# Performance work log

Hardware: AMD Instinct MI355X
Metric: run time of the kernel (lower is better)

Reference implementation:

```python
import jax, jax.numpy as jnp
import numpy as np

DIM = 1024
NUM_HEADS = 16
HEAD_DIM = DIM // NUM_HEADS
FF = 4 * DIM
B, T, S = 8, 512, 4096


def setup_inputs() -> dict:
    key = jax.random.key(0)
    ks = jax.random.split(key, 14)
    sc = 1.0 / np.sqrt(DIM)
    inp = {
        "x": jax.random.normal(ks[0], (B, T, DIM), jnp.float32),
        "inp": jax.random.normal(ks[1], (B, S, DIM), jnp.float32),
        # attention projections
        "Wq": jax.random.normal(ks[2], (DIM, DIM), jnp.float32) * sc,
        "bq": jnp.zeros((DIM,), jnp.float32),
        "Wk": jax.random.normal(ks[3], (DIM, DIM), jnp.float32) * sc,
        "bk": jnp.zeros((DIM,), jnp.float32),
        "Wv": jax.random.normal(ks[4], (DIM, DIM), jnp.float32) * sc,
        "bv": jnp.zeros((DIM,), jnp.float32),
        "Wo": jax.random.normal(ks[5], (DIM, DIM), jnp.float32) * sc,
        "bo": jnp.zeros((DIM,), jnp.float32),
        # MLP
        "W1": jax.random.normal(ks[6], (DIM, FF), jnp.float32) * sc,
        "b1": jnp.zeros((FF,), jnp.float32),
        "W2": jax.random.normal(ks[7], (FF, DIM), jnp.float32) * (1.0 / np.sqrt(FF)),
        "b2": jnp.zeros((DIM,), jnp.float32),
    }
    return inp


def _perceiver_layer(x, inp, Wq, bq, Wk, bk, Wv, bv, Wo, bo, W1, b1, W2, b2):
    b, t, _ = x.shape
    s = inp.shape[1]
    q = (x @ Wq + bq).reshape(b, t, NUM_HEADS, HEAD_DIM)
    k = (inp @ Wk + bk).reshape(b, s, NUM_HEADS, HEAD_DIM)
    v = (inp @ Wv + bv).reshape(b, s, NUM_HEADS, HEAD_DIM)
    # [b, h, t, s] score tensor (as in original code)
    attn = jnp.einsum('bthd,bshd->bhts', q, k)
    attn = jax.nn.softmax(attn / jnp.sqrt(jnp.float32(HEAD_DIM)), axis=-1)
    out = jnp.einsum('bhts,bshd->bthd', attn, v).reshape(b, t, DIM)
    attn_out = out @ Wo + bo
    x = x + attn_out
    h = jax.nn.gelu(x @ W1 + b1, approximate=True)  # flax nn.gelu default is tanh approx
    x = x + (h @ W2 + b2)
    return x


def reference(x, inp, Wq, bq, Wk, bk, Wv, bv, Wo, bo, W1, b1, W2, b2):
    return _perceiver_layer(x, inp, Wq, bq, Wk, bk, Wv, bv, Wo, bo, W1, b1, W2, b2)
```

## Files before the change

kernel.cpp:

```cpp
#include <hip/hip_runtime.h>
#include <hip/hip_bf16.h>

#define DIM 1024
#define NHEADS 16
#define HDIM 64
#define FF_ 4096
#define BB 8
#define TT 512
#define SS 4096

typedef __attribute__((ext_vector_type(8))) __bf16 bf16x8;
typedef __attribute__((ext_vector_type(4))) float f32x4;
typedef __attribute__((ext_vector_type(4))) unsigned short us4;

#define SWZ(r, b) ((b) ^ (((r) & 7) << 4))

typedef const __attribute__((address_space(1))) void gvoid_t;
typedef __attribute__((address_space(3))) void lvoid_t;

__device__ __forceinline__ void ldst16(const void* g, void* l) {
  __builtin_amdgcn_global_load_lds((gvoid_t*)g, (lvoid_t*)l, 16, 0, 0);
}

__device__ inline unsigned short f2bf(float f) {
  unsigned u = __float_as_uint(f);
  u += 0x7fff + ((u >> 16) & 1);
  return (unsigned short)(u >> 16);
}

__device__ __forceinline__ unsigned cvt_pk(float lo, float hi) {
  unsigned r;
  asm("v_cvt_pk_bf16_f32 %0, %1, %2" : "=v"(r) : "v"(lo), "v"(hi));
  return r;
}

__global__ void prep_kernel(const float* __restrict__ x,
                            const float* __restrict__ inp,
                            const float* __restrict__ Wq,
                            const float* __restrict__ Wk,
                            const float* __restrict__ Wv,
                            const float* __restrict__ Wo,
                            const float* __restrict__ W1,
                            const float* __restrict__ W2,
                            const float* __restrict__ bk,
                            const float* __restrict__ bv,
                            unsigned short* __restrict__ xb,
                            unsigned short* __restrict__ inpb,
                            unsigned short* __restrict__ Wqt,
                            unsigned short* __restrict__ Wkvt,
                            unsigned short* __restrict__ Wot,
                            unsigned short* __restrict__ W1t,
                            unsigned short* __restrict__ W2t,
                            float* __restrict__ bkv) {
  __shared__ float tile[32][33];
  const int bid = blockIdx.x, tid = threadIdx.x;

  if (bid < 2048) {
    const int n4 = BB * SS * DIM / 4;
    for (int i = bid * 256 + tid; i < n4; i += 2048 * 256) {
      float4 v = ((const float4*)inp)[i];
      uint2 w = {cvt_pk(v.x, v.y), cvt_pk(v.z, v.w)};
      ((uint2*)inpb)[i] = w;
    }
    return;
  }
  if (bid < 2304) {
    const int n4 = BB * TT * DIM / 4;
    for (int i = (bid - 2048) * 256 + tid; i < n4; i += 256 * 256) {
      float4 v = ((const float4*)x)[i];
      uint2 w = {cvt_pk(v.x, v.y), cvt_pk(v.z, v.w)};
      ((uint2*)xb)[i] = w;
    }
    return;
  }
  if (bid < 14592) {
    const float* in;
    unsigned short* outp;
    int R, C, t, tilesx;
    if (bid < 3328)       { in = Wq; outp = Wqt; R = 1024; C = 1024; t = bid - 2304; tilesx = 32; }
    else if (bid < 4352)  { in = Wk; outp = Wkvt; R = 1024; C = 1024; t = bid - 3328; tilesx = 32; }
    else if (bid < 5376)  { in = Wv; outp = Wkvt + 1024 * 1024; R = 1024; C = 1024; t = bid - 4352; tilesx = 32; }
    else if (bid < 6400)  { in = Wo; outp = Wot; R = 1024; C = 1024; t = bid - 5376; tilesx = 32; }
    else if (bid < 10496) { in = W1; outp = W1t; R = 1024; C = 4096; t = bid - 6400; tilesx = 128; }
    else                  { in = W2; outp = W2t; R = 4096; C = 1024; t = bid - 10496; tilesx = 32; }
    int bc = (t % tilesx) * 32, br = (t / tilesx) * 32;
    int tx = tid & 31, ty = tid >> 5;
#pragma unroll
    for (int i = 0; i < 32; i += 8)
      tile[ty + i][tx] = in[(size_t)(br + ty + i) * C + bc + tx];
    __syncthreads();
#pragma unroll
    for (int i = 0; i < 32; i += 8)
      outp[(size_t)(bc + ty + i) * R + br + tx] = f2bf(tile[tx][ty + i]);
    return;
  }
  for (int i = tid; i < 1024; i += 256) {
    bkv[i] = bk[i];
    bkv[1024 + i] = bv[i];
  }
}

template <int EPI>
__global__ __launch_bounds__(256, 3)
void gemm_kernel(const unsigned short* __restrict__ A,
                 const unsigned short* __restrict__ Bt,
                 const float* __restrict__ bias,
                 const float* __restrict__ res,
                 void* __restrict__ Cp,
                 unsigned short* __restrict__ C2,
                 int M, int N, int K) {
  __shared__ char smem[32768];
  char* As = smem;
  char* Bs = smem + 16384;

  const int tid = threadIdx.x;
  const int lane = tid & 63;
  const int wave = tid >> 6;
  const int wm = wave >> 1, wn = wave & 1;

  const int flat = blockIdx.y * gridDim.x + blockIdx.x;
  const int cpx = (gridDim.x * gridDim.y) >> 3;
  const int swz = (flat & 7) * cpx + (flat >> 3);
  const int m0 = (swz / gridDim.x) * 128, n0 = (swz % gridDim.x) * 128;

  f32x4 acc[4][4];
#pragma unroll
  for (int i = 0; i < 4; ++i)
#pragma unroll
    for (int j = 0; j < 4; ++j) acc[i][j] = (f32x4){0.f, 0.f, 0.f, 0.f};

  for (int k0 = 0; k0 < K; k0 += 64) {
    __syncthreads();
#pragma unroll
    for (int i = 0; i < 4; ++i) {
      int ch = (wave * 4 + i) * 64 + lane;
      int r = ch >> 3, c8 = (ch & 7) ^ (r & 7);
      ldst16(A + (size_t)(m0 + r) * K + k0 + c8 * 8, As + (wave * 4 + i) * 1024);
      ldst16(Bt + (size_t)(n0 + r) * K + k0 + c8 * 8, Bs + (wave * 4 + i) * 1024);
    }
    __syncthreads();

#pragma unroll
    for (int kk = 0; kk < 2; ++kk) {
      bf16x8 a[4], b[4];
#pragma unroll
      for (int mi = 0; mi < 4; ++mi) {
        int r = wm * 64 + mi * 16 + (lane & 15);
        a[mi] = *(const bf16x8*)(As + r * 128 + SWZ(r, kk * 64 + (lane >> 4) * 16));
      }
#pragma unroll
      for (int ni = 0; ni < 4; ++ni) {
        int r = wn * 64 + ni * 16 + (lane & 15);
        b[ni] = *(const bf16x8*)(Bs + r * 128 + SWZ(r, kk * 64 + (lane >> 4) * 16));
      }
#pragma unroll
      for (int mi = 0; mi < 4; ++mi)
#pragma unroll
        for (int ni = 0; ni < 4; ++ni)
          acc[mi][ni] = __builtin_amdgcn_mfma_f32_16x16x32_bf16(b[ni], a[mi], acc[mi][ni], 0, 0, 0);
    }
  }

  const int q = lane & 15, g4 = (lane >> 4) * 4;
#pragma unroll
  for (int mi = 0; mi < 4; ++mi) {
    int row = m0 + wm * 64 + mi * 16 + q;
#pragma unroll
    for (int ni = 0; ni < 4; ++ni) {
      int colb = n0 + wn * 64 + ni * 16 + g4;
      float4 bv = *(const float4*)(bias + colb);
      f32x4 v = acc[mi][ni];
      float v0 = v[0] + bv.x, v1 = v[1] + bv.y, v2 = v[2] + bv.z, v3 = v[3] + bv.w;
      if (EPI == 0) {
        uint2 w = {cvt_pk(v0, v1), cvt_pk(v2, v3)};
        *(uint2*)((unsigned short*)Cp + (size_t)row * N + colb) = w;
      } else if (EPI == 1) {
        float o[4] = {v0, v1, v2, v3};
#pragma unroll
        for (int j = 0; j < 4; ++j) {
          float u = 0.7978845608028654f * (o[j] + 0.044715f * o[j] * o[j] * o[j]);
          float e = __expf(2.f * u);
          float th = 1.f - 2.f / (e + 1.f);
          o[j] = 0.5f * o[j] * (1.f + th);
        }
        uint2 w = {cvt_pk(o[0], o[1]), cvt_pk(o[2], o[3])};
        *(uint2*)((unsigned short*)Cp + (size_t)row * N + colb) = w;
      } else {
        float4 r4 = *(const float4*)(res + (size_t)row * N + colb);
        float o0 = v0 + r4.x, o1 = v1 + r4.y, o2 = v2 + r4.z, o3 = v3 + r4.w;
        float4 ov = {o0, o1, o2, o3};
        *(float4*)((float*)Cp + (size_t)row * N + colb) = ov;
        if (EPI == 3) {
          uint2 w = {cvt_pk(o0, o1), cvt_pk(o2, o3)};
          *(uint2*)(C2 + (size_t)row * N + colb) = w;
        }
      }
    }
  }
}

template <int EPI>
__global__ __launch_bounds__(512, 2)
void gemm256(const unsigned short* __restrict__ A,
             const unsigned short* __restrict__ Bt,
             const float* __restrict__ bias,
             void* __restrict__ Cp,
             unsigned short* __restrict__ C2,
             int M, int N, int K) {
  __shared__ char smem[131072];

  const int tid = threadIdx.x, lane = tid & 63, wave = tid >> 6;
  const int q = lane & 15, g = lane >> 4;
  const int wm = wave >> 2, wn = wave & 3;

  const int flat = blockIdx.y * gridDim.x + blockIdx.x;
  const int cpx = (gridDim.x * gridDim.y) >> 3;
  const int swz = (flat & 7) * cpx + (flat >> 3);
  const int m0 = (swz / gridDim.x) * 256, n0 = (swz % gridDim.x) * 256;

  const unsigned short* Arow = A + (size_t)m0 * K;
  const unsigned short* Brow = Bt + (size_t)n0 * K;

  const int r0 = tid >> 3, c0 = ((tid & 7) ^ (r0 & 7)) * 8;
  const int r1 = (tid + 512) >> 3, c1 = (((tid + 512) & 7) ^ (r1 & 7)) * 8;

#define STA(buf, half, kt)                                                     \
  { char* d = smem + (buf) * 32768 + (half) * 16384;                           \
    const unsigned short* s = Arow + (size_t)((half) * 128) * K + (kt) * 64;   \
    ldst16(s + (size_t)r0 * K + c0, d + tid * 16);                             \
    ldst16(s + (size_t)r1 * K + c1, d + 8192 + tid * 16); }
#define STB(buf, half, kt)                                                     \
  { char* d = smem + 65536 + (buf) * 32768 + (half) * 16384;                   \
    const unsigned short* s = Brow + (size_t)((half) * 128) * K + (kt) * 64;   \
    ldst16(s + (size_t)r0 * K + c0, d + tid * 16);                             \
    ldst16(s + (size_t)r1 * K + c1, d + 8192 + tid * 16); }

  f32x4 acc[8][4];
#pragma unroll
  for (int i = 0; i < 8; ++i)
#pragma unroll
    for (int j = 0; j < 4; ++j) acc[i][j] = (f32x4){0.f, 0.f, 0.f, 0.f};

  STA(0, 0, 0); STA(0, 1, 0); STB(0, 0, 0); STB(0, 1, 0);
  STB(1, 0, 1); STB(1, 1, 1);
  asm volatile("s_waitcnt vmcnt(4)" ::: "memory");
  __builtin_amdgcn_s_barrier();

  const int NKT = K >> 6;
  for (int kt = 0; kt < NKT; ++kt) {
    const int cb = kt & 1, nb = cb ^ 1;
    const char* Ab = smem + cb * 32768;
    const char* Bb = smem + 65536 + cb * 32768;
    bf16x8 bfr[4][2];

#pragma unroll
    for (int p = 0; p < 4; ++p) {
      bf16x8 af[2][2];
#pragma unroll
      for (int i = 0; i < 2; ++i)
#pragma unroll
        for (int kk = 0; kk < 2; ++kk) {
          int r = wm * 128 + (2 * p + i) * 16 + q;
          af[i][kk] = *(const bf16x8*)(Ab + r * 128 + SWZ(r, kk * 64 + g * 16));
        }
      if (p == 0) {
#pragma unroll
        for (int nr = 0; nr < 4; ++nr)
#pragma unroll
          for (int kk = 0; kk < 2; ++kk) {
            int r = wn * 64 + nr * 16 + q;
            bfr[nr][kk] = *(const bf16x8*)(Bb + r * 128 + SWZ(r, kk * 64 + g * 16));
          }
      }

      if (p == 0)      { if (kt + 1 < NKT) { STA(nb, 0, kt + 1); STA(nb, 1, kt + 1); } }
      else if (p == 1) { if (kt + 2 < NKT) STB(cb, 0, kt + 2); }
      else if (p == 2) { if (kt + 2 < NKT) STB(cb, 1, kt + 2); }

      __builtin_amdgcn_s_barrier();
      __builtin_amdgcn_s_setprio(1);
#pragma unroll
      for (int i = 0; i < 2; ++i)
#pragma unroll
        for (int nr = 0; nr < 4; ++nr)
#pragma unroll
          for (int kk = 0; kk < 2; ++kk)
            acc[2 * p + i][nr] = __builtin_amdgcn_mfma_f32_16x16x32_bf16(
                bfr[nr][kk], af[i][kk], acc[2 * p + i][nr], 0, 0, 0);
      __builtin_amdgcn_s_setprio(0);

      if (p == 3) {
        if (kt + 2 < NKT) { asm volatile("s_waitcnt vmcnt(4)" ::: "memory"); }
        else              { asm volatile("s_waitcnt vmcnt(0)" ::: "memory"); }
      }
      __builtin_amdgcn_s_barrier();
    }
  }

  const int g4 = g * 4;
#pragma unroll
  for (int mr = 0; mr < 8; ++mr) {
    int row = m0 + wm * 128 + mr * 16 + q;
#pragma unroll
    for (int nr = 0; nr < 4; ++nr) {
      int colb = n0 + wn * 64 + nr * 16 + g4;
      float4 bv = *(const float4*)(bias + colb);
      f32x4 v = acc[mr][nr];
      float v0 = v[0] + bv.x, v1 = v[1] + bv.y, v2 = v[2] + bv.z, v3 = v[3] + bv.w;
      if (EPI == 1) {
        float o[4] = {v0, v1, v2, v3};
#pragma unroll
        for (int j = 0; j < 4; ++j) {
          float u = 0.7978845608028654f * (o[j] + 0.044715f * o[j] * o[j] * o[j]);
          float e = __expf(2.f * u);
          float th = 1.f - 2.f / (e + 1.f);
          o[j] = 0.5f * o[j] * (1.f + th);
        }
        uint2 w = {cvt_pk(o[0], o[1]), cvt_pk(o[2], o[3])};
        *(uint2*)((unsigned short*)Cp + (size_t)row * N + colb) = w;
      } else {
        if (n0 < 1024) {
          uint2 w = {cvt_pk(v0, v1), cvt_pk(v2, v3)};
          *(uint2*)((unsigned short*)Cp + (size_t)row * 1024 + colb) = w;
        } else {
          int b = row >> 12, s = row & 4095;
          int d0 = colb - 1024;
          unsigned short* vt = C2 + ((size_t)b * DIM + d0) * SS + s;
          vt[0] = f2bf(v0);
          vt[SS] = f2bf(v1);
          vt[2 * SS] = f2bf(v2);
          vt[3 * SS] = f2bf(v3);
        }
      }
    }
  }
#undef STA
#undef STB
}

__global__ __launch_bounds__(256, 2)
void attn_kernel6(const unsigned short* __restrict__ Qb,
                  const unsigned short* __restrict__ Kb,
                  const unsigned short* __restrict__ Vt,
                  unsigned short* __restrict__ Ob) {
  __shared__ char smem[65536];

  const int tid = threadIdx.x, lane = tid & 63, wave = tid >> 6;
  const int bid = blockIdx.x;
  const int b = bid & 7, qt = (bid >> 3) & 3, h = bid >> 5;
  const int q0 = qt * 128;
  const int q = lane & 15, g = lane >> 4;

  const int rA = tid >> 3;
  const int cA = (tid & 7) ^ (rA & 7);
  char* const Pw = smem + 49152 + wave * 4096;

  const unsigned short* srcQ = Qb + ((size_t)b * TT + q0) * DIM + h * HDIM;
  const unsigned short* srcK = Kb + (size_t)b * SS * DIM + h * HDIM;
  const unsigned short* srcV = Vt + ((size_t)b * DIM + h * HDIM) * SS;

  bf16x8 qf0[2], qf1[2];
  {
    const unsigned short* qr0 = srcQ + (size_t)(wave * 32 + q) * DIM;
    const unsigned short* qr1 = srcQ + (size_t)(wave * 32 + 16 + q) * DIM;
    qf0[0] = *(const bf16x8*)(qr0 + g * 8);
    qf0[1] = *(const bf16x8*)(qr0 + 32 + g * 8);
    qf1[0] = *(const bf16x8*)(qr1 + g * 8);
    qf1[1] = *(const bf16x8*)(qr1 + 32 + g * 8);
  }

#define STKV(t, buf)                                                                        \
  { ldst16(srcK + (size_t)((t) * 64 + rA) * DIM + cA * 8, smem + (buf) * 8192 + tid * 16);  \
    ldst16(srcK + (size_t)((t) * 64 + rA + 32) * DIM + cA * 8,                              \
           smem + (buf) * 8192 + 4096 + tid * 16);                                          \
    ldst16(srcV + (size_t)rA * SS + (t) * 64 + cA * 8,                                      \
           smem + 24576 + (buf) * 8192 + tid * 16);                                         \
    ldst16(srcV + (size_t)(rA + 32) * SS + (t) * 64 + cA * 8,                               \
           smem + 24576 + (buf) * 8192 + 4096 + tid * 16); }

  STKV(0, 0);
  STKV(1, 1);
  asm volatile("s_waitcnt vmcnt(4)" ::: "memory");
  __builtin_amdgcn_s_barrier();

  f32x4 acc0[4], acc1[4];
#pragma unroll
  for (int dt = 0; dt < 4; ++dt) {
    acc0[dt] = (f32x4){0.f, 0.f, 0.f, 0.f};
    acc1[dt] = (f32x4){0.f, 0.f, 0.f, 0.f};
  }
  float lsum0 = 0.f, lsum1 = 0.f;
  const float CSC = 0.125f * 1.4426950408889634f;

  const int NT = SS / 64;
  int cur = 0, sb = 2;
  for (int t = 0; t < NT; ++t) {
    char* Kc = smem + cur * 8192;
    char* Vc = smem + 24576 + cur * 8192;
    if (t + 2 < NT) STKV(t + 2, sb);

    f32x4 st0[4], st1[4];
#pragma unroll
    for (int si = 0; si < 4; ++si) {
      st0[si] = (f32x4){0.f, 0.f, 0.f, 0.f};
      st1[si] = (f32x4){0.f, 0.f, 0.f, 0.f};
    }
    __builtin_amdgcn_s_setprio(1);
#pragma unroll
    for (int kk = 0; kk < 2; ++kk)
#pragma unroll
      for (int si = 0; si < 4; ++si) {
        int r = si * 16 + q;
        bf16x8 kf = *(const bf16x8*)(Kc + r * 128 + SWZ(r, kk * 64 + g * 16));
        st0[si] = __builtin_amdgcn_mfma_f32_16x16x32_bf16(kf, qf0[kk], st0[si], 0, 0, 0);
        st1[si] = __builtin_amdgcn_mfma_f32_16x16x32_bf16(kf, qf1[kk], st1[si], 0, 0, 0);
      }
    __builtin_amdgcn_s_setprio(0);

    float rs0 = 0.f, rs1 = 0.f;
#pragma unroll
    for (int si = 0; si < 4; ++si) {
      float a0 = __builtin_amdgcn_exp2f(st0[si][0] * CSC);
      float a1 = __builtin_amdgcn_exp2f(st0[si][1] * CSC);
      float a2 = __builtin_amdgcn_exp2f(st0[si][2] * CSC);
      float a3 = __builtin_amdgcn_exp2f(st0[si][3] * CSC);
      rs0 += (a0 + a1) + (a2 + a3);
      uint2 w0 = {cvt_pk(a0, a1), cvt_pk(a2, a3)};
      *(uint2*)(Pw + q * 128 + SWZ(q, si * 32 + g * 8)) = w0;
      float b0 = __builtin_amdgcn_exp2f(st1[si][0] * CSC);
      float b1 = __builtin_amdgcn_exp2f(st1[si][1] * CSC);
      float b2 = __builtin_amdgcn_exp2f(st1[si][2] * CSC);
      float b3 = __builtin_amdgcn_exp2f(st1[si][3] * CSC);
      rs1 += (b0 + b1) + (b2 + b3);
      uint2 w1 = {cvt_pk(b0, b1), cvt_pk(b2, b3)};
      *(uint2*)(Pw + 2048 + q * 128 + SWZ(q, si * 32 + g * 8)) = w1;
    }
    lsum0 += rs0;
    lsum1 += rs1;

    __builtin_amdgcn_s_setprio(1);
#pragma unroll
    for (int kk = 0; kk < 2; ++kk) {
      bf16x8 pb0 = *(const bf16x8*)(Pw + q * 128 + SWZ(q, kk * 64 + g * 16));
      bf16x8 pb1 = *(const bf16x8*)(Pw + 2048 + q * 128 + SWZ(q, kk * 64 + g * 16));
#pragma unroll
      for (int dt = 0; dt < 4; ++dt) {
        int r = dt * 16 + q;
        bf16x8 va = *(const bf16x8*)(Vc + r * 128 + SWZ(r, kk * 64 + g * 16));
        acc0[dt] = __builtin_amdgcn_mfma_f32_16x16x32_bf16(va, pb0, acc0[dt], 0, 0, 0);
        acc1[dt] = __builtin_amdgcn_mfma_f32_16x16x32_bf16(va, pb1, acc1[dt], 0, 0, 0);
      }
    }
    __builtin_amdgcn_s_setprio(0);

    if (t + 2 < NT) { asm volatile("s_waitcnt vmcnt(4)" ::: "memory"); }
    else            { asm volatile("s_waitcnt vmcnt(0)" ::: "memory"); }
    __builtin_amdgcn_s_barrier();
    cur = cur == 2 ? 0 : cur + 1;
    sb  = sb  == 2 ? 0 : sb  + 1;
  }
#undef STKV

  lsum0 += __shfl_xor(lsum0, 16);
  lsum0 += __shfl_xor(lsum0, 32);
  lsum1 += __shfl_xor(lsum1, 16);
  lsum1 += __shfl_xor(lsum1, 32);
  float inv0 = 1.0f / lsum0, inv1 = 1.0f / lsum1;
#pragma unroll
  for (int dt = 0; dt < 4; ++dt) {
    f32x4 v0 = acc0[dt];
    uint2 w0 = {cvt_pk(v0[0] * inv0, v0[1] * inv0), cvt_pk(v0[2] * inv0, v0[3] * inv0)};
    *(uint2*)(Pw + q * 128 + SWZ(q, dt * 32 + g * 8)) = w0;
    f32x4 v1 = acc1[dt];
    uint2 w1 = {cvt_pk(v1[0] * inv1, v1[1] * inv1), cvt_pk(v1[2] * inv1, v1[3] * inv1)};
    *(uint2*)(Pw + 2048 + q * 128 + SWZ(q, dt * 32 + g * 8)) = w1;
  }
  __builtin_amdgcn_s_waitcnt(0);
  int qr = lane >> 2, cb = (lane & 3) * 32;
  {
    uint4 lo = *(const uint4*)(Pw + qr * 128 + SWZ(qr, cb));
    uint4 hi = *(const uint4*)(Pw + qr * 128 + SWZ(qr, cb + 16));
    size_t ob = ((size_t)b * TT + q0 + wave * 32 + qr) * DIM + h * HDIM + (lane & 3) * 16;
    *(uint4*)(Ob + ob) = lo;
    *(uint4*)(Ob + ob + 8) = hi;
  }
  {
    uint4 lo = *(const uint4*)(Pw + 2048 + qr * 128 + SWZ(qr, cb));
    uint4 hi = *(const uint4*)(Pw + 2048 + qr * 128 + SWZ(qr, cb + 16));
    size_t ob = ((size_t)b * TT + q0 + wave * 32 + 16 + qr) * DIM + h * HDIM + (lane & 3) * 16;
    *(uint4*)(Ob + ob) = lo;
    *(uint4*)(Ob + ob + 8) = hi;
  }
}

extern "C" void kernel_launch(void* const* d_in, const int* in_sizes, int n_in,
                              void* d_out, int out_size, void* d_ws, size_t ws_size,
                              hipStream_t stream) {
  const float* x   = (const float*)d_in[0];
  const float* inp = (const float*)d_in[1];
  const float* Wq  = (const float*)d_in[2];
  const float* bq  = (const float*)d_in[3];
  const float* Wk  = (const float*)d_in[4];
  const float* bk  = (const float*)d_in[5];
  const float* Wv  = (const float*)d_in[6];
  const float* bv  = (const float*)d_in[7];
  const float* Wo  = (const float*)d_in[8];
  const float* bo  = (const float*)d_in[9];
  const float* W1  = (const float*)d_in[10];
  const float* b1  = (const float*)d_in[11];
  const float* W2  = (const float*)d_in[12];
  const float* b2  = (const float*)d_in[13];
  float* out = (float*)d_out;

  char* ws = (char*)d_ws;
  const size_t MB = 1024ull * 1024ull;
  unsigned short* Wqt  = (unsigned short*)(ws + 0 * MB);
  unsigned short* Wkvt = (unsigned short*)(ws + 2 * MB);
  unsigned short* Wot  = (unsigned short*)(ws + 6 * MB);
  unsigned short* W1t  = (unsigned short*)(ws + 8 * MB);
  unsigned short* W2t  = (unsigned short*)(ws + 16 * MB);
  float*          bkv  = (float*)(ws + 24 * MB);
  unsigned short* Qb   = (unsigned short*)(ws + 25 * MB);
  unsigned short* Kb   = (unsigned short*)(ws + 33 * MB);
  float*          x2   = (float*)(ws + 33 * MB);
  unsigned short* x2b  = (unsigned short*)(ws + 49 * MB);
  unsigned short* hb   = (unsigned short*)(ws + 57 * MB);
  unsigned short* Vt   = (unsigned short*)(ws + 97 * MB);
  unsigned short* inpb = (unsigned short*)(ws + 161 * MB);
  unsigned short* xb   = (unsigned short*)(ws + 225 * MB);
  unsigned short* Obf  = (unsigned short*)d_out;

  prep_kernel<<<dim3(14593), 256, 0, stream>>>(x, inp, Wq, Wk, Wv, Wo, W1, W2,
                                               bk, bv, xb, inpb, Wqt, Wkvt,
                                               Wot, W1t, W2t, bkv);

  gemm_kernel<0><<<dim3(8, 32), 256, 0, stream>>>(xb, Wqt, bq, nullptr, Qb, nullptr, BB * TT, DIM, DIM);
  gemm256<2><<<dim3(8, 128), 512, 0, stream>>>(inpb, Wkvt, bkv, Kb, Vt, BB * SS, 2048, DIM);

  attn_kernel6<<<dim3(512), 256, 0, stream>>>(Qb, Kb, Vt, Obf);

  gemm_kernel<3><<<dim3(8, 32), 256, 0, stream>>>(Obf, Wot, bo, x, x2, x2b, BB * TT, DIM, DIM);
  gemm256<1><<<dim3(16, 16), 512, 0, stream>>>(x2b, W1t, b1, hb, nullptr, BB * TT, FF_, DIM);
  gemm_kernel<2><<<dim3(8, 32), 256, 0, stream>>>(hb, W2t, b2, x2, out, nullptr, BB * TT, DIM, FF_);
}
```

Baseline: 452.7 us.

## Switch attention kernel to 32x32x16 MFMA with register-resident P via lane shuffles

The attention kernel now uses 32x32x16 bf16 MFMA tiles instead of 16x16x32 for both QK^T and PV. The exponentiated scores are packed in registers and exchanged across half-waves with shuffles to form the PV operand, so P no longer round-trips through LDS each tile. This is meant to cut LDS traffic, LDS reads and MFMA instruction count per tile. In exchange it adds cross-lane shuffles and selects in the inner loop, and relies on the 32x32 accumulator layout matching the operand layout.

Result: no change. 459.6 us (+1.5%).

```diff
diff --git a/kernel.cpp b/kernel.cpp
--- a/kernel.cpp
+++ b/kernel.cpp
@@ -11,6 +11,7 @@
 
 typedef __attribute__((ext_vector_type(8))) __bf16 bf16x8;
 typedef __attribute__((ext_vector_type(4))) float f32x4;
+typedef __attribute__((ext_vector_type(16))) float f32x16;
 typedef __attribute__((ext_vector_type(4))) unsigned short us4;
 
 #define SWZ(r, b) ((b) ^ (((r) & 7) << 4))
@@ -339,7 +340,7 @@
 }
 
 __global__ __launch_bounds__(256, 2)
-void attn_kernel6(const unsigned short* __restrict__ Qb,
+void attn_kernel7(const unsigned short* __restrict__ Qb,
                   const unsigned short* __restrict__ Kb,
                   const unsigned short* __restrict__ Vt,
                   unsigned short* __restrict__ Ob) {
@@ -349,7 +350,9 @@
   const int bid = blockIdx.x;
   const int b = bid & 7, qt = (bid >> 3) & 3, h = bid >> 5;
   const int q0 = qt * 128;
-  const int q = lane & 15, g = lane >> 4;
+  const int q = lane & 31;
+  const bool hi = lane >= 32;
+  const int ho16 = hi ? 16 : 0;
 
   const int rA = tid >> 3;
   const int cA = (tid & 7) ^ (rA & 7);
@@ -359,14 +362,11 @@
   const unsigned short* srcK = Kb + (size_t)b * SS * DIM + h * HDIM;
   const unsigned short* srcV = Vt + ((size_t)b * DIM + h * HDIM) * SS;
 
-  bf16x8 qf0[2], qf1[2];
+  bf16x8 qf[4];
   {
-    const unsigned short* qr0 = srcQ + (size_t)(wave * 32 + q) * DIM;
-    const unsigned short* qr1 = srcQ + (size_t)(wave * 32 + 16 + q) * DIM;
-    qf0[0] = *(const bf16x8*)(qr0 + g * 8);
-    qf0[1] = *(const bf16x8*)(qr0 + 32 + g * 8);
-    qf1[0] = *(const bf16x8*)(qr1 + g * 8);
-    qf1[1] = *(const bf16x8*)(qr1 + 32 + g * 8);
+    const unsigned short* qrow = srcQ + (size_t)(wave * 32 + q) * DIM + (hi ? 8 : 0);
+#pragma unroll
+    for (int dt = 0; dt < 4; ++dt) qf[dt] = *(const bf16x8*)(qrow + dt * 16);
   }
 
 #define STKV(t, buf)                                                                        \
@@ -383,13 +383,10 @@
   asm volatile("s_waitcnt vmcnt(4)" ::: "memory");
   __builtin_amdgcn_s_barrier();
 
-  f32x4 acc0[4], acc1[4];
-#pragma unroll
-  for (int dt = 0; dt < 4; ++dt) {
-    acc0[dt] = (f32x4){0.f, 0.f, 0.f, 0.f};
-    acc1[dt] = (f32x4){0.f, 0.f, 0.f, 0.f};
-  }
-  float lsum0 = 0.f, lsum1 = 0.f;
+  f32x16 oa0, oa1;
+#pragma unroll
+  for (int i = 0; i < 16; ++i) { oa0[i] = 0.f; oa1[i] = 0.f; }
+  float lsum = 0.f;
   const float CSC = 0.125f * 1.4426950408889634f;
 
   const int NT = SS / 64;
@@ -399,57 +396,56 @@
     char* Vc = smem + 24576 + cur * 8192;
     if (t + 2 < NT) STKV(t + 2, sb);
 
-    f32x4 st0[4], st1[4];
-#pragma unroll
-    for (int si = 0; si < 4; ++si) {
-      st0[si] = (f32x4){0.f, 0.f, 0.f, 0.f};
-      st1[si] = (f32x4){0.f, 0.f, 0.f, 0.f};
-    }
+    f32x16 sa0, sa1;
+#pragma unroll
+    for (int i = 0; i < 16; ++i) { sa0[i] = 0.f; sa1[i] = 0.f; }
     __builtin_amdgcn_s_setprio(1);
 #pragma unroll
-    for (int kk = 0; kk < 2; ++kk)
-#pragma unroll
-      for (int si = 0; si < 4; ++si) {
-        int r = si * 16 + q;
-        bf16x8 kf = *(const bf16x8*)(Kc + r * 128 + SWZ(r, kk * 64 + g * 16));
-        st0[si] = __builtin_amdgcn_mfma_f32_16x16x32_bf16(kf, qf0[kk], st0[si], 0, 0, 0);
-        st1[si] = __builtin_amdgcn_mfma_f32_16x16x32_bf16(kf, qf1[kk], st1[si], 0, 0, 0);
-      }
+    for (int dt = 0; dt < 4; ++dt) {
+      bf16x8 kf0 = *(const bf16x8*)(Kc + q * 128 + SWZ(q, dt * 32 + ho16));
+      bf16x8 kf1 = *(const bf16x8*)(Kc + (32 + q) * 128 + SWZ(32 + q, dt * 32 + ho16));
+      sa0 = __builtin_amdgcn_mfma_f32_32x32x16_bf16(kf0, qf[dt], sa0, 0, 0, 0);
+      sa1 = __builtin_amdgcn_mfma_f32_32x32x16_bf16(kf1, qf[dt], sa1, 0, 0, 0);
+    }
     __builtin_amdgcn_s_setprio(0);
 
-    float rs0 = 0.f, rs1 = 0.f;
-#pragma unroll
-    for (int si = 0; si < 4; ++si) {
-      float a0 = __builtin_amdgcn_exp2f(st0[si][0] * CSC);
-      float a1 = __builtin_amdgcn_exp2f(st0[si][1] * CSC);
-      float a2 = __builtin_amdgcn_exp2f(st0[si][2] * CSC);
-      float a3 = __builtin_amdgcn_exp2f(st0[si][3] * CSC);
-      rs0 += (a0 + a1) + (a2 + a3);
-      uint2 w0 = {cvt_pk(a0, a1), cvt_pk(a2, a3)};
-      *(uint2*)(Pw + q * 128 + SWZ(q, si * 32 + g * 8)) = w0;
-      float b0 = __builtin_amdgcn_exp2f(st1[si][0] * CSC);
-      float b1 = __builtin_amdgcn_exp2f(st1[si][1] * CSC);
-      float b2 = __builtin_amdgcn_exp2f(st1[si][2] * CSC);
-      float b3 = __builtin_amdgcn_exp2f(st1[si][3] * CSC);
-      rs1 += (b0 + b1) + (b2 + b3);
-      uint2 w1 = {cvt_pk(b0, b1), cvt_pk(b2, b3)};
-      *(uint2*)(Pw + 2048 + q * 128 + SWZ(q, si * 32 + g * 8)) = w1;
-    }
-    lsum0 += rs0;
-    lsum1 += rs1;
+    float rs = 0.f;
+    unsigned W0[8], W1[8];
+#pragma unroll
+    for (int m = 0; m < 8; ++m) {
+      float a0 = __builtin_amdgcn_exp2f(sa0[2 * m] * CSC);
+      float a1 = __builtin_amdgcn_exp2f(sa0[2 * m + 1] * CSC);
+      float b0 = __builtin_amdgcn_exp2f(sa1[2 * m] * CSC);
+      float b1 = __builtin_amdgcn_exp2f(sa1[2 * m + 1] * CSC);
+      rs += (a0 + a1) + (b0 + b1);
+      W0[m] = cvt_pk(a0, a1);
+      W1[m] = cvt_pk(b0, b1);
+    }
+    lsum += rs;
 
     __builtin_amdgcn_s_setprio(1);
 #pragma unroll
-    for (int kk = 0; kk < 2; ++kk) {
-      bf16x8 pb0 = *(const bf16x8*)(Pw + q * 128 + SWZ(q, kk * 64 + g * 16));
-      bf16x8 pb1 = *(const bf16x8*)(Pw + 2048 + q * 128 + SWZ(q, kk * 64 + g * 16));
-#pragma unroll
-      for (int dt = 0; dt < 4; ++dt) {
-        int r = dt * 16 + q;
-        bf16x8 va = *(const bf16x8*)(Vc + r * 128 + SWZ(r, kk * 64 + g * 16));
-        acc0[dt] = __builtin_amdgcn_mfma_f32_16x16x32_bf16(va, pb0, acc0[dt], 0, 0, 0);
-        acc1[dt] = __builtin_amdgcn_mfma_f32_16x16x32_bf16(va, pb1, acc1[dt], 0, 0, 0);
-      }
+    for (int st = 0; st < 4; ++st) {
+      const int j = 4 * (st & 1);
+      unsigned a0 = (st < 2) ? W0[j] : W1[j];
+      unsigned a1 = (st < 2) ? W0[j + 1] : W1[j + 1];
+      unsigned a2 = (st < 2) ? W0[j + 2] : W1[j + 2];
+      unsigned a3 = (st < 2) ? W0[j + 3] : W1[j + 3];
+      unsigned T0 = hi ? a0 : a2;
+      unsigned T1 = hi ? a1 : a3;
+      unsigned R0 = __shfl_xor(T0, 32);
+      unsigned R1 = __shfl_xor(T1, 32);
+      uint4 u;
+      u.x = hi ? R0 : a0;
+      u.y = hi ? R1 : a1;
+      u.z = hi ? a2 : R0;
+      u.w = hi ? a3 : R1;
+      bf16x8 pb;
+      __builtin_memcpy(&pb, &u, 16);
+      bf16x8 vf0 = *(const bf16x8*)(Vc + q * 128 + SWZ(q, st * 32 + ho16));
+      bf16x8 vf1 = *(const bf16x8*)(Vc + (32 + q) * 128 + SWZ(32 + q, st * 32 + ho16));
+      oa0 = __builtin_amdgcn_mfma_f32_32x32x16_bf16(vf0, pb, oa0, 0, 0, 0);
+      oa1 = __builtin_amdgcn_mfma_f32_32x32x16_bf16(vf1, pb, oa1, 0, 0, 0);
     }
     __builtin_amdgcn_s_setprio(0);
 
@@ -461,35 +457,31 @@
   }
 #undef STKV
 
-  lsum0 += __shfl_xor(lsum0, 16);
-  lsum0 += __shfl_xor(lsum0, 32);
-  lsum1 += __shfl_xor(lsum1, 16);
-  lsum1 += __shfl_xor(lsum1, 32);
-  float inv0 = 1.0f / lsum0, inv1 = 1.0f / lsum1;
-#pragma unroll
-  for (int dt = 0; dt < 4; ++dt) {
-    f32x4 v0 = acc0[dt];
-    uint2 w0 = {cvt_pk(v0[0] * inv0, v0[1] * inv0), cvt_pk(v0[2] * inv0, v0[3] * inv0)};
-    *(uint2*)(Pw + q * 128 + SWZ(q, dt * 32 + g * 8)) = w0;
-    f32x4 v1 = acc1[dt];
-    uint2 w1 = {cvt_pk(v1[0] * inv1, v1[1] * inv1), cvt_pk(v1[2] * inv1, v1[3] * inv1)};
-    *(uint2*)(Pw + 2048 + q * 128 + SWZ(q, dt * 32 + g * 8)) = w1;
+  lsum += __shfl_xor(lsum, 32);
+  float inv = 1.0f / lsum;
+#pragma unroll
+  for (int d32 = 0; d32 < 2; ++d32) {
+#pragma unroll
+    for (int rq = 0; rq < 4; ++rq) {
+      int dbase = d32 * 32 + (hi ? 4 : 0) + 8 * rq;
+      float o0 = (d32 ? oa1[4 * rq] : oa0[4 * rq]) * inv;
+      float o1 = (d32 ? oa1[4 * rq + 1] : oa0[4 * rq + 1]) * inv;
+      float o2 = (d32 ? oa1[4 * rq + 2] : oa0[4 * rq + 2]) * inv;
+      float o3 = (d32 ? oa1[4 * rq + 3] : oa0[4 * rq + 3]) * inv;
+      uint2 w = {cvt_pk(o0, o1), cvt_pk(o2, o3)};
+      *(uint2*)(Pw + q * 128 + SWZ(q, dbase * 2)) = w;
+    }
   }
   __builtin_amdgcn_s_waitcnt(0);
-  int qr = lane >> 2, cb = (lane & 3) * 32;
-  {
-    uint4 lo = *(const uint4*)(Pw + qr * 128 + SWZ(qr, cb));
-    uint4 hi = *(const uint4*)(Pw + qr * 128 + SWZ(qr, cb + 16));
-    size_t ob = ((size_t)b * TT + q0 + wave * 32 + qr) * DIM + h * HDIM + (lane & 3) * 16;
+  int qr = lane >> 2, cb2 = (lane & 3) * 32;
+#pragma unroll
+  for (int half = 0; half < 2; ++half) {
+    int row = half * 16 + qr;
+    uint4 lo = *(const uint4*)(Pw + row * 128 + SWZ(row, cb2));
+    uint4 hi4 = *(const uint4*)(Pw + row * 128 + SWZ(row, cb2 + 16));
+    size_t ob = ((size_t)b * TT + q0 + wave * 32 + row) * DIM + h * HDIM + (lane & 3) * 16;
     *(uint4*)(Ob + ob) = lo;
-    *(uint4*)(Ob + ob + 8) = hi;
-  }
-  {
-    uint4 lo = *(const uint4*)(Pw + 2048 + qr * 128 + SWZ(qr, cb));
-    uint4 hi = *(const uint4*)(Pw + 2048 + qr * 128 + SWZ(qr, cb + 16));
-    size_t ob = ((size_t)b * TT + q0 + wave * 32 + 16 + qr) * DIM + h * HDIM + (lane & 3) * 16;
-    *(uint4*)(Ob + ob) = lo;
-    *(uint4*)(Ob + ob + 8) = hi;
+    *(uint4*)(Ob + ob + 8) = hi4;
   }
 }
 
@@ -537,7 +529,7 @@
   gemm_kernel<0><<<dim3(8, 32), 256, 0, stream>>>(xb, Wqt, bq, nullptr, Qb, nullptr, BB * TT, DIM, DIM);
   gemm256<2><<<dim3(8, 128), 512, 0, stream>>>(inpb, Wkvt, bkv, Kb, Vt, BB * SS, 2048, DIM);
 
-  attn_kernel6<<<dim3(512), 256, 0, stream>>>(Qb, Kb, Vt, Obf);
+  attn_kernel7<<<dim3(512), 256, 0, stream>>>(Qb, Kb, Vt, Obf);
 
   gemm_kernel<3><<<dim3(8, 32), 256, 0, stream>>>(Obf, Wot, bo, x, x2, x2b, BB * TT, DIM, DIM);
   gemm256<1><<<dim3(16, 16), 512, 0, stream>>>(x2b, W1t, b1, hb, nullptr, BB * TT, FF_, DIM);
```
